# Kernel optimization log

Hardware: AMD Instinct MI355X
Metric: run time of the kernel (lower is better)

## Reference

```python
import jax, jax.numpy as jnp
import numpy as np

D_MODEL = 512
NUM_HEADS = 8
D_QKV = D_MODEL // NUM_HEADS  # 64
CAPACITY = 2  # EUNN tunable-style rotation layers per step
B = 2
L = 256


def setup_inputs() -> dict:
    key = jax.random.key(0)
    ks = jax.random.split(key, 16)
    f = jnp.float32
    x_q = jax.random.normal(ks[0], (B, L, D_MODEL), f)
    x_k = jax.random.normal(ks[1], (B, L, D_MODEL), f)
    x_v = jax.random.normal(ks[2], (B, L, D_MODEL), f)
    mask = jnp.zeros((B, 1, L, L), f)
    s = 1.0 / np.sqrt(D_MODEL).astype(np.float32)
    Wq = jax.random.normal(ks[3], (D_MODEL, D_MODEL), f) * s
    Wk = jax.random.normal(ks[4], (D_MODEL, D_MODEL), f) * s
    Wv = jax.random.normal(ks[5], (D_MODEL, D_MODEL), f) * s
    Wo = jax.random.normal(ks[6], (D_MODEL, D_MODEL), f) * s
    bq = jnp.zeros((D_MODEL,), f); bk = jnp.zeros((D_MODEL,), f)
    bv = jnp.zeros((D_MODEL,), f); bo = jnp.zeros((D_MODEL,), f)
    pi = np.float32(np.pi)
    theta = jax.random.uniform(ks[7], (NUM_HEADS, CAPACITY, D_QKV // 2), f, -pi, pi)
    phi = jax.random.uniform(ks[8], (NUM_HEADS, CAPACITY, D_QKV // 2), f, -pi, pi)
    sw = 1.0 / np.sqrt(D_QKV).astype(np.float32)
    Win_re = jax.random.normal(ks[9], (NUM_HEADS, D_QKV, D_QKV), f) * sw
    Win_im = jax.random.normal(ks[10], (NUM_HEADS, D_QKV, D_QKV), f) * sw
    rnn_bias = jax.random.normal(ks[11], (NUM_HEADS, D_QKV), f) * 0.01
    return dict(x_q=x_q, x_k=x_k, x_v=x_v, mask=mask, Wq=Wq, bq=bq, Wk=Wk, bk=bk,
                Wv=Wv, bv=bv, Wo=Wo, bo=bo, theta=theta, phi=phi,
                Win_re=Win_re, Win_im=Win_im, rnn_bias=rnn_bias)


def _apply_unitary(h, theta, phi):
    # h: [B,H,Q,d] complex64. EUNN unitary = product of Givens-rotation layers,
    # alternating even pairings (0,1),(2,3),.. and odd pairings via roll.
    for c in range(theta.shape[1]):
        if c % 2 == 1:
            h = jnp.roll(h, -1, axis=-1)
        sh = h.shape
        hp = h.reshape(sh[:-1] + (sh[-1] // 2, 2))
        a, b = hp[..., 0], hp[..., 1]
        cs = jnp.cos(theta[:, c, :])[None, :, None, :]
        sn = jnpp_sin = jnp.sin(theta[:, c, :])[None, :, None, :]
        ph = jnp.exp(1j * phi[:, c, :].astype(jnp.complex64))[None, :, None, :]
        na = cs * a - (sn * ph) * b
        nb = (sn * jnp.conj(ph)) * a + cs * b
        h = jnp.stack([na, nb], axis=-1).reshape(sh)
        if c % 2 == 1:
            h = jnp.roll(h, 1, axis=-1)
    return h


def _modrelu(z, b):
    m = jnp.abs(z)
    scale = jax.nn.relu(m + b) / (m + 1e-5)
    return z * scale.astype(z.dtype)


def _forward(x_q, x_k, x_v, mask, Wq, bq, Wk, bk, Wv, bv, Wo, bo,
             theta, phi, Win_re, Win_im, rnn_bias):
    Bm, Lq, _ = x_q.shape
    def heads(x):
        return x.reshape(Bm, -1, NUM_HEADS, D_QKV).transpose(0, 2, 1, 3)
    q = heads(x_q @ Wq + bq)   # [B,H,Lq,d]
    k = heads(x_k @ Wk + bk)   # [B,H,Lk,d]
    v = heads(x_v @ Wv + bv)   # [B,H,Lk,d]
    logits = jnp.einsum('bhqd,bhkd->bhqk', q, k) / jnp.sqrt(jnp.float32(D_QKV))
    logits = logits - jnp.where(mask == 1.0, jnp.inf, mask)
    attn = jax.nn.softmax(logits, axis=-1)  # [B,H,Lq,Lk]
    Win = (Win_re + 1j * Win_im).astype(jnp.complex64)  # [H,d,d]
    bb = rnn_bias[None, :, None, :]
    def step(h, xs):
        a_t, v_t = xs                              # [B,H,Q], [B,H,d]
        x_t = a_t[..., None] * v_t[:, :, None, :]  # [B,H,Q,d] streamed weighted value
        wx = jnp.einsum('bhqd,hde->bhqe', x_t.astype(jnp.complex64), Win)
        return _modrelu(_apply_unitary(h, theta, phi) + wx, bb), None
    h0 = jnp.zeros((Bm, NUM_HEADS, Lq, D_QKV), jnp.complex64)
    xs = (attn.transpose(3, 0, 1, 2), v.transpose(2, 0, 1, 3))
    hT, _ = jax.lax.scan(step, h0, xs)
    rnn_out = jnp.real(hT)  # [B,H,Lq,d] -- TF takes final RNN state, real part
    out = rnn_out.transpose(0, 2, 1, 3).reshape(Bm, Lq, D_MODEL) @ Wo + bo
    return out, attn


def reference(x_q, x_k, x_v, mask, Wq, bq, Wk, bk, Wv, bv, Wo, bo,
              theta, phi, Win_re, Win_im, rnn_bias):
    return _forward(x_q, x_k, x_v, mask, Wq, bq, Wk, bk, Wv, bv, Wo, bo,
                    theta, phi, Win_re, Win_im, rnn_bias)
```

## Files before the change

kernel.cpp:

```cpp
#include <hip/hip_runtime.h>
#include <math.h>

#define NB 2
#define NL 256
#define DM 512
#define NH 8
#define DQ 64

typedef float v2f __attribute__((ext_vector_type(2)));

#if __has_builtin(__builtin_elementwise_fma)
__device__ __forceinline__ v2f fmav(v2f a, v2f b, v2f c) {
    return __builtin_elementwise_fma(a, b, c);
}
#else
__device__ __forceinline__ v2f fmav(v2f a, v2f b, v2f c) {
    v2f r; r.x = fmaf(a.x, b.x, c.x); r.y = fmaf(a.y, b.y, c.y); return r;
}
#endif
__device__ __forceinline__ v2f swapv(v2f a) {
    return __builtin_shufflevector(a, a, 1, 0);
}

__global__ __launch_bounds__(256) void qkv_gemm(
    const float* __restrict__ xq, const float* __restrict__ xk,
    const float* __restrict__ xv,
    const float* __restrict__ Wq, const float* __restrict__ Wk,
    const float* __restrict__ Wv,
    const float* __restrict__ bq, const float* __restrict__ bk,
    const float* __restrict__ bv,
    const float* __restrict__ Wre, const float* __restrict__ Wim,
    float* __restrict__ q, float* __restrict__ kT, float2* __restrict__ u)
{
    int z = blockIdx.z;
    const float* X = (z == 0) ? xq : (z == 1) ? xk : xv;
    const float* W = (z == 0) ? Wq : (z == 1) ? Wk : Wv;
    const float* bias = (z == 0) ? bq : (z == 1) ? bk : bv;

    __shared__ float As[32][33];
    __shared__ float Bs[32][68];

    int tid = threadIdx.x;
    int tx = tid & 15, ty = tid >> 4;
    int m0 = blockIdx.y * 32, n0 = blockIdx.x * 64;

    int ar = tid >> 3, ac4 = (tid & 7) * 4;
    int br = tid >> 4, bc4 = (tid & 15) * 4;
    const float* Aptr = X + (m0 + ar) * 512 + ac4;
    const float* Bptr0 = W + br * 512 + n0 + bc4;
    const float* Bptr1 = W + (br + 16) * 512 + n0 + bc4;

    float acc[2][4] = {};

    float4 aR = *(const float4*)(Aptr);
    float4 bR0 = *(const float4*)(Bptr0);
    float4 bR1 = *(const float4*)(Bptr1);

    for (int k0 = 0; k0 < 512; k0 += 32) {
        As[ac4 + 0][ar] = aR.x; As[ac4 + 1][ar] = aR.y;
        As[ac4 + 2][ar] = aR.z; As[ac4 + 3][ar] = aR.w;
        *(float4*)&Bs[br][bc4] = bR0;
        *(float4*)&Bs[br + 16][bc4] = bR1;
        __syncthreads();

        if (k0 + 32 < 512) {
            aR  = *(const float4*)(Aptr + k0 + 32);
            bR0 = *(const float4*)(Bptr0 + (k0 + 32) * 512);
            bR1 = *(const float4*)(Bptr1 + (k0 + 32) * 512);
        }

        #pragma unroll
        for (int kk = 0; kk < 32; kk++) {
            float a0 = As[kk][ty * 2 + 0];
            float a1 = As[kk][ty * 2 + 1];
            float4 bb = *(const float4*)&Bs[kk][tx * 4];
            acc[0][0] += a0 * bb.x; acc[0][1] += a0 * bb.y;
            acc[0][2] += a0 * bb.z; acc[0][3] += a0 * bb.w;
            acc[1][0] += a1 * bb.x; acc[1][1] += a1 * bb.y;
            acc[1][2] += a1 * bb.z; acc[1][3] += a1 * bb.w;
        }
        __syncthreads();
    }

    if (z < 2) {
        float* O = (z == 0) ? q : kT;
        #pragma unroll
        for (int i = 0; i < 2; i++) {
            int m = m0 + ty * 2 + i;
            int b = m >> 8, l = m & 255;
            #pragma unroll
            for (int j = 0; j < 4; j++) {
                int n = n0 + tx * 4 + j;
                int h = n >> 6, d = n & 63;
                float val = acc[i][j] + bias[n];
                if (z == 1)
                    O[((b * NH + h) * DQ + d) * NL + l] = val;
                else
                    O[((b * NH + h) * NL + l) * DQ + d] = val;
            }
        }
    } else {
        int h = blockIdx.x;
        int b = m0 >> 8;
        #pragma unroll
        for (int i = 0; i < 2; i++)
            #pragma unroll
            for (int j = 0; j < 4; j++)
                Bs[ty * 2 + i][tx * 4 + j] = acc[i][j] + bias[n0 + tx * 4 + j];
        __syncthreads();

        int r0 = ty * 2, c4 = tx * 4;
        float ur[2][4] = {}, ui[2][4] = {};
        const float* wr = Wre + h * 4096 + c4;
        const float* wi = Wim + h * 4096 + c4;
        #pragma unroll 4
        for (int d = 0; d < 64; d++) {
            float v0 = Bs[r0][d];
            float v1 = Bs[r0 + 1][d];
            float4 wre = *(const float4*)(wr + d * 64);
            float4 wim = *(const float4*)(wi + d * 64);
            ur[0][0] += v0 * wre.x; ur[0][1] += v0 * wre.y;
            ur[0][2] += v0 * wre.z; ur[0][3] += v0 * wre.w;
            ui[0][0] += v0 * wim.x; ui[0][1] += v0 * wim.y;
            ui[0][2] += v0 * wim.z; ui[0][3] += v0 * wim.w;
            ur[1][0] += v1 * wre.x; ur[1][1] += v1 * wre.y;
            ur[1][2] += v1 * wre.z; ur[1][3] += v1 * wre.w;
            ui[1][0] += v1 * wim.x; ui[1][1] += v1 * wim.y;
            ui[1][2] += v1 * wim.z; ui[1][3] += v1 * wim.w;
        }
        #pragma unroll
        for (int i = 0; i < 2; i++) {
            int l = (m0 & 255) + r0 + i;
            float2* up = u + ((size_t)(b * NH + h) * NL + l) * DQ + c4;
            #pragma unroll
            for (int j = 0; j < 4; j++)
                up[j] = make_float2(ur[i][j], ui[i][j]);
        }
    }
}

__device__ __forceinline__ float dpp_row_ror1(float x) {
    return __int_as_float(__builtin_amdgcn_mov_dpp(__float_as_int(x), 0x121, 0xF, 0xF, true));
}
__device__ __forceinline__ float dpp_row_rol1(float x) {
    return __int_as_float(__builtin_amdgcn_mov_dpp(__float_as_int(x), 0x12F, 0xF, 0xF, true));
}

__device__ __forceinline__ v2f mdr(v2f z, float bv) {
    float mm = z.x * z.x + z.y * z.y;
    float m = __builtin_amdgcn_sqrtf(mm);
    float sc = fmaxf(m + bv, 0.f) * __builtin_amdgcn_rcpf(m + 1e-5f);
    v2f s = {sc, sc};
    return z * s;
}

__global__ __launch_bounds__(64) void rnn_kernel(
    const float* __restrict__ q, const float* __restrict__ kT,
    const float* __restrict__ mask, float* __restrict__ attn_o,
    const float2* __restrict__ u,
    const float* __restrict__ theta, const float* __restrict__ phi,
    const float* __restrict__ rnn_bias, float* __restrict__ rnn_out)
{
    int lane = threadIdx.x;
    int blk = blockIdx.x;
    int qg = blk & 63;
    int h  = (blk >> 6) & 7;
    int b  = blk >> 9;

    int row = lane >> 4;
    int p   = lane & 15;

    __shared__ float qs[4][68];
    __shared__ float arow[4][260];

    {
        const float4* qsrc = (const float4*)(q + ((size_t)(b * NH + h) * NL + qg * 4) * DQ);
        float4 f4 = qsrc[lane];
        *(float4*)&qs[lane >> 4][(lane & 15) * 4] = f4;
    }
    __syncthreads();

    float l[4][4];
    {
        const float* kp = kT + (size_t)((b * NH + h) * DQ) * NL + lane;
        float acc[4][4] = {};
        #pragma unroll
        for (int d4 = 0; d4 < 16; d4++) {
            float kv[4][4];
            #pragma unroll
            for (int kk = 0; kk < 4; kk++)
                #pragma unroll
                for (int i = 0; i < 4; i++)
                    kv[kk][i] = kp[(size_t)(d4 * 4 + i) * NL + kk * 64];
            #pragma unroll
            for (int r = 0; r < 4; r++) {
                float4 qv = *(const float4*)&qs[r][d4 * 4];
                #pragma unroll
                for (int kk = 0; kk < 4; kk++)
                    acc[r][kk] += qv.x * kv[kk][0] + qv.y * kv[kk][1]
                                + qv.z * kv[kk][2] + qv.w * kv[kk][3];
            }
        }
        #pragma unroll
        for (int r = 0; r < 4; r++)
            #pragma unroll
            for (int kk = 0; kk < 4; kk++) {
                float mv = mask[(size_t)(b * NL + qg * 4 + r) * NL + lane + kk * 64];
                l[r][kk] = acc[r][kk] * 0.125f - ((mv == 1.0f) ? INFINITY : mv);
            }
        #pragma unroll
        for (int r = 0; r < 4; r++) {
            float mx = fmaxf(fmaxf(l[r][0], l[r][1]), fmaxf(l[r][2], l[r][3]));
            #pragma unroll
            for (int o = 32; o; o >>= 1) mx = fmaxf(mx, __shfl_xor(mx, o, 64));
            float s = __expf(l[r][0] - mx) + __expf(l[r][1] - mx)
                    + __expf(l[r][2] - mx) + __expf(l[r][3] - mx);
            #pragma unroll
            for (int o = 32; o; o >>= 1) s += __shfl_xor(s, o, 64);
            float rs = __builtin_amdgcn_rcpf(s);
            #pragma unroll
            for (int kk = 0; kk < 4; kk++) {
                float pv = __expf(l[r][kk] - mx) * rs;
                attn_o[((size_t)(b * NH + h) * NL + qg * 4 + r) * NL + lane + kk * 64] = pv;
                arow[r][lane + kk * 64] = pv;
            }
        }
    }
    __syncthreads();

    const float* tb = theta + h * 64;
    const float* pb = phi + h * 64;

    float thA = tb[2 * p], phA = pb[2 * p];
    float cA = cosf(thA), sA = sinf(thA), cpA = cosf(phA), spA = sinf(phA);
    float thB = tb[2 * p + 1], phB = pb[2 * p + 1];
    float cB = cosf(thB), sB = sinf(thB), cpB = cosf(phB), spB = sinf(phB);

    #define MKC(nm, Wr, Wi) v2f nm##rV = {(Wr), (Wr)}; v2f nm##iN = {-(Wi), (Wi)}
    MKC(WAa, -sA * cpA, -sA * spA);
    MKC(WAb,  sA * cpA, -sA * spA);
    MKC(WBa, -sB * cpB, -sB * spB);
    MKC(WBb,  sB * cpB, -sB * spB);
    v2f cAv = {cA, cA}, cBv = {cB, cB};

    int iL = (2 * p + 31) & 31;
    float thL = tb[32 + iL], phL = pb[32 + iL];
    float cL = cosf(thL), sL = sinf(thL);
    MKC(W1L,  sL * cosf(phL), -sL * sinf(phL));
    float thM = tb[32 + 2 * p], phM = pb[32 + 2 * p];
    float cM = cosf(thM), sM = sinf(thM), cpM = cosf(phM), spM = sinf(phM);
    MKC(W1M, -sM * cpM, -sM * spM);
    MKC(W2M,  sM * cpM, -sM * spM);
    float thR = tb[32 + 2 * p + 1], phR = pb[32 + 2 * p + 1];
    float cR = cosf(thR), sR = sinf(thR);
    MKC(W1R, -sR * cosf(phR), -sR * sinf(phR));
    v2f cLv = {cL, cL}, cMv = {cM, cM}, cRv = {cR, cR};
    #undef MKC

    float4 bias4 = *(const float4*)&rnn_bias[h * 64 + 4 * p];

    v2f e0 = {0.f, 0.f}, e1 = {0.f, 0.f}, e2 = {0.f, 0.f}, e3 = {0.f, 0.f};

    #define STEP(a_t, uA, uB) do {                                           \
        v2f atv = {(a_t), (a_t)};                                            \
        v2f u0 = {(uA).x, (uA).y}, u1 = {(uA).z, (uA).w};                    \
        v2f u2 = {(uB).x, (uB).y}, u3 = {(uB).z, (uB).w};                    \
        v2f g0 = fmav(cAv, e0, fmav(WAarV, e1, WAaiN * swapv(e1)));          \
        v2f g1 = fmav(cAv, e1, fmav(WAbrV, e0, WAbiN * swapv(e0)));          \
        v2f g2 = fmav(cBv, e2, fmav(WBarV, e3, WBaiN * swapv(e3)));          \
        v2f g3 = fmav(cBv, e3, fmav(WBbrV, e2, WBbiN * swapv(e2)));          \
        v2f gl, gr;                                                          \
        gl.x = dpp_row_ror1(g3.x); gl.y = dpp_row_ror1(g3.y);                \
        gr.x = dpp_row_rol1(g0.x); gr.y = dpp_row_rol1(g0.y);                \
        v2f z0 = fmav(cLv, g0, fmav(W1LrV, gl, fmav(W1LiN, swapv(gl), atv * u0))); \
        v2f z1 = fmav(cMv, g1, fmav(W1MrV, g2, fmav(W1MiN, swapv(g2), atv * u1))); \
        v2f z2 = fmav(cMv, g2, fmav(W2MrV, g1, fmav(W2MiN, swapv(g1), atv * u2))); \
        v2f z3 = fmav(cRv, g3, fmav(W1RrV, gr, fmav(W1RiN, swapv(gr), atv * u3))); \
        e0 = mdr(z0, bias4.x); e1 = mdr(z1, bias4.y);                        \
        e2 = mdr(z2, bias4.z); e3 = mdr(z3, bias4.w);                        \
    } while (0)

    const float4* up4 = (const float4*)(u + (size_t)((b * NH + h) * NL) * DQ) + 2 * p;

    float4 Ua[8], Ub[8];
    float4 aa, ab;
    #pragma unroll
    for (int i = 0; i < 8; i++) Ua[i] = up4[(i >> 1) * 32 + (i & 1)];
    aa = *(const float4*)&arow[row][0];

    for (int c = 0; c < 64; c += 2) {
        const float4* upn = up4 + (c + 1) * 128;
        #pragma unroll
        for (int i = 0; i < 8; i++) Ub[i] = upn[(i >> 1) * 32 + (i & 1)];
        ab = *(const float4*)&arow[row][(c + 1) * 4];

        STEP(aa.x, Ua[0], Ua[1]);
        STEP(aa.y, Ua[2], Ua[3]);
        STEP(aa.z, Ua[4], Ua[5]);
        STEP(aa.w, Ua[6], Ua[7]);

        if (c + 2 < 64) {
            const float4* upn2 = up4 + (c + 2) * 128;
            #pragma unroll
            for (int i = 0; i < 8; i++) Ua[i] = upn2[(i >> 1) * 32 + (i & 1)];
            aa = *(const float4*)&arow[row][(c + 2) * 4];
        }

        STEP(ab.x, Ub[0], Ub[1]);
        STEP(ab.y, Ub[2], Ub[3]);
        STEP(ab.z, Ub[4], Ub[5]);
        STEP(ab.w, Ub[6], Ub[7]);
    }
    #undef STEP

    int qi = qg * 4 + row;
    float4 o4 = {e0.x, e1.x, e2.x, e3.x};
    *(float4*)&rnn_out[(size_t)(b * NL + qi) * DM + h * DQ + 4 * p] = o4;
}

__global__ __launch_bounds__(256) void out_gemm(
    const float* __restrict__ A, const float* __restrict__ W,
    const float* __restrict__ bias, float* __restrict__ C)
{
    __shared__ float As[32][17];
    __shared__ float Bs[32][68];

    int tid = threadIdx.x;
    int tx = tid & 15, ty = tid >> 4;
    int m0 = blockIdx.y * 16, n0 = blockIdx.x * 64;

    int ar = tid >> 4, ac2 = (tid & 15) * 2;
    int br = tid >> 4, bc4 = (tid & 15) * 4;
    const float* Aptr = A + (m0 + ar) * 512 + ac2;
    const float* Bptr0 = W + br * 512 + n0 + bc4;
    const float* Bptr1 = W + (br + 16) * 512 + n0 + bc4;

    float acc[4] = {};

    float2 aR = *(const float2*)(Aptr);
    float4 bR0 = *(const float4*)(Bptr0);
    float4 bR1 = *(const float4*)(Bptr1);

    for (int k0 = 0; k0 < 512; k0 += 32) {
        As[ac2 + 0][ar] = aR.x; As[ac2 + 1][ar] = aR.y;
        *(float4*)&Bs[br][bc4] = bR0;
        *(float4*)&Bs[br + 16][bc4] = bR1;
        __syncthreads();

        if (k0 + 32 < 512) {
            aR  = *(const float2*)(Aptr + k0 + 32);
            bR0 = *(const float4*)(Bptr0 + (k0 + 32) * 512);
            bR1 = *(const float4*)(Bptr1 + (k0 + 32) * 512);
        }

        #pragma unroll
        for (int kk = 0; kk < 32; kk++) {
            float a = As[kk][ty];
            float4 bb = *(const float4*)&Bs[kk][tx * 4];
            acc[0] += a * bb.x; acc[1] += a * bb.y;
            acc[2] += a * bb.z; acc[3] += a * bb.w;
        }
        __syncthreads();
    }

    int m = m0 + ty;
    #pragma unroll
    for (int j = 0; j < 4; j++) {
        int n = n0 + tx * 4 + j;
        C[m * 512 + n] = acc[j] + bias[n];
    }
}

extern "C" void kernel_launch(void* const* d_in, const int* in_sizes, int n_in,
                              void* d_out, int out_size, void* d_ws, size_t ws_size,
                              hipStream_t stream)
{
    const float* x_q  = (const float*)d_in[0];
    const float* x_k  = (const float*)d_in[1];
    const float* x_v  = (const float*)d_in[2];
    const float* mask = (const float*)d_in[3];
    const float* Wq   = (const float*)d_in[4];
    const float* bq   = (const float*)d_in[5];
    const float* Wk   = (const float*)d_in[6];
    const float* bk   = (const float*)d_in[7];
    const float* Wv   = (const float*)d_in[8];
    const float* bv   = (const float*)d_in[9];
    const float* Wo   = (const float*)d_in[10];
    const float* bo   = (const float*)d_in[11];
    const float* theta= (const float*)d_in[12];
    const float* phi  = (const float*)d_in[13];
    const float* Wre  = (const float*)d_in[14];
    const float* Wim  = (const float*)d_in[15];
    const float* rb   = (const float*)d_in[16];

    float* ws = (float*)d_ws;
    float*  q_ws    = ws;
    float*  kT_ws   = ws + 262144;
    float2* u_ws    = (float2*)(ws + 524288);
    float*  rnn_o   = ws + 1048576;

    float* out_o  = (float*)d_out;
    float* attn_o = out_o + NB * NL * DM;

    qkv_gemm<<<dim3(8, 16, 3), 256, 0, stream>>>(
        x_q, x_k, x_v, Wq, Wk, Wv, bq, bk, bv, Wre, Wim,
        q_ws, kT_ws, u_ws);

    rnn_kernel<<<dim3(1024), 64, 0, stream>>>(
        q_ws, kT_ws, mask, attn_o, u_ws, theta, phi, rb, rnn_o);

    out_gemm<<<dim3(8, 32), 256, 0, stream>>>(rnn_o, Wo, bo, out_o);
}
```

Baseline: 182.0 us.

## Halve per-lane RNN state and double blocks in recurrent kernel

The RNN kernel now handles 2 query rows per 64-lane block instead of 4, so each lane carries 2 complex state elements (one Givens pair) rather than 4. The grid doubles to 2048 blocks. The cross-lane shift for the odd rotation layer becomes two DPP quad-perm moves over interleaved lanes instead of a row rotate. The aim is to shorten the serial 256-step per-lane dependency chain and raise parallelism, at the cost of recomputing the QK logits and loading K once per 2 rows instead of once per 4.

```diff
diff --git a/kernel.cpp b/kernel.cpp
--- a/kernel.cpp
+++ b/kernel.cpp
@@ -139,11 +139,15 @@
     }
 }
 
-__device__ __forceinline__ float dpp_row_ror1(float x) {
-    return __int_as_float(__builtin_amdgcn_mov_dpp(__float_as_int(x), 0x121, 0xF, 0xF, true));
-}
-__device__ __forceinline__ float dpp_row_rol1(float x) {
-    return __int_as_float(__builtin_amdgcn_mov_dpp(__float_as_int(x), 0x12F, 0xF, 0xF, true));
+__device__ __forceinline__ float rot_up2(float x) {
+    int v = __builtin_amdgcn_mov_dpp(__float_as_int(x), 0x134, 0xF, 0xF, true);
+    v = __builtin_amdgcn_mov_dpp(v, 0x134, 0xF, 0xF, true);
+    return __int_as_float(v);
+}
+__device__ __forceinline__ float rot_dn2(float x) {
+    int v = __builtin_amdgcn_mov_dpp(__float_as_int(x), 0x13C, 0xF, 0xF, true);
+    v = __builtin_amdgcn_mov_dpp(v, 0x13C, 0xF, 0xF, true);
+    return __int_as_float(v);
 }
 
 __device__ __forceinline__ v2f mdr(v2f z, float bv) {
@@ -163,27 +167,28 @@
 {
     int lane = threadIdx.x;
     int blk = blockIdx.x;
-    int qg = blk & 63;
-    int h  = (blk >> 6) & 7;
-    int b  = blk >> 9;
-
-    int row = lane >> 4;
-    int p   = lane & 15;
-
-    __shared__ float qs[4][68];
-    __shared__ float arow[4][260];
+    int qg = blk & 127;
+    int h  = (blk >> 7) & 7;
+    int b  = blk >> 10;
+
+    int row = lane & 1;
+    int p   = lane >> 1;
+
+    __shared__ float qs[2][68];
+    __shared__ float arow[2][260];
 
     {
-        const float4* qsrc = (const float4*)(q + ((size_t)(b * NH + h) * NL + qg * 4) * DQ);
-        float4 f4 = qsrc[lane];
-        *(float4*)&qs[lane >> 4][(lane & 15) * 4] = f4;
+        const float4* qsrc = (const float4*)(q + ((size_t)(b * NH + h) * NL + qg * 2) * DQ);
+        if (lane < 32) {
+            float4 f4 = qsrc[lane];
+            *(float4*)&qs[lane >> 4][(lane & 15) * 4] = f4;
+        }
     }
     __syncthreads();
 
-    float l[4][4];
     {
         const float* kp = kT + (size_t)((b * NH + h) * DQ) * NL + lane;
-        float acc[4][4] = {};
+        float acc[2][4] = {};
         #pragma unroll
         for (int d4 = 0; d4 < 16; d4++) {
             float kv[4][4];
@@ -193,7 +198,7 @@
                 for (int i = 0; i < 4; i++)
                     kv[kk][i] = kp[(size_t)(d4 * 4 + i) * NL + kk * 64];
             #pragma unroll
-            for (int r = 0; r < 4; r++) {
+            for (int r = 0; r < 2; r++) {
                 float4 qv = *(const float4*)&qs[r][d4 * 4];
                 #pragma unroll
                 for (int kk = 0; kk < 4; kk++)
@@ -201,15 +206,16 @@
                                 + qv.z * kv[kk][2] + qv.w * kv[kk][3];
             }
         }
-        #pragma unroll
-        for (int r = 0; r < 4; r++)
+        float l[2][4];
+        #pragma unroll
+        for (int r = 0; r < 2; r++)
             #pragma unroll
             for (int kk = 0; kk < 4; kk++) {
-                float mv = mask[(size_t)(b * NL + qg * 4 + r) * NL + lane + kk * 64];
+                float mv = mask[(size_t)(b * NL + qg * 2 + r) * NL + lane + kk * 64];
                 l[r][kk] = acc[r][kk] * 0.125f - ((mv == 1.0f) ? INFINITY : mv);
             }
         #pragma unroll
-        for (int r = 0; r < 4; r++) {
+        for (int r = 0; r < 2; r++) {
             float mx = fmaxf(fmaxf(l[r][0], l[r][1]), fmaxf(l[r][2], l[r][3]));
             #pragma unroll
             for (int o = 32; o; o >>= 1) mx = fmaxf(mx, __shfl_xor(mx, o, 64));
@@ -221,7 +227,7 @@
             #pragma unroll
             for (int kk = 0; kk < 4; kk++) {
                 float pv = __expf(l[r][kk] - mx) * rs;
-                attn_o[((size_t)(b * NH + h) * NL + qg * 4 + r) * NL + lane + kk * 64] = pv;
+                attn_o[((size_t)(b * NH + h) * NL + qg * 2 + r) * NL + lane + kk * 64] = pv;
                 arow[r][lane + kk * 64] = pv;
             }
         }
@@ -231,91 +237,78 @@
     const float* tb = theta + h * 64;
     const float* pb = phi + h * 64;
 
-    float thA = tb[2 * p], phA = pb[2 * p];
-    float cA = cosf(thA), sA = sinf(thA), cpA = cosf(phA), spA = sinf(phA);
-    float thB = tb[2 * p + 1], phB = pb[2 * p + 1];
-    float cB = cosf(thB), sB = sinf(thB), cpB = cosf(phB), spB = sinf(phB);
-
     #define MKC(nm, Wr, Wi) v2f nm##rV = {(Wr), (Wr)}; v2f nm##iN = {-(Wi), (Wi)}
-    MKC(WAa, -sA * cpA, -sA * spA);
-    MKC(WAb,  sA * cpA, -sA * spA);
-    MKC(WBa, -sB * cpB, -sB * spB);
-    MKC(WBb,  sB * cpB, -sB * spB);
-    v2f cAv = {cA, cA}, cBv = {cB, cB};
-
-    int iL = (2 * p + 31) & 31;
-    float thL = tb[32 + iL], phL = pb[32 + iL];
-    float cL = cosf(thL), sL = sinf(thL);
-    MKC(W1L,  sL * cosf(phL), -sL * sinf(phL));
-    float thM = tb[32 + 2 * p], phM = pb[32 + 2 * p];
-    float cM = cosf(thM), sM = sinf(thM), cpM = cosf(phM), spM = sinf(phM);
-    MKC(W1M, -sM * cpM, -sM * spM);
-    MKC(W2M,  sM * cpM, -sM * spM);
-    float thR = tb[32 + 2 * p + 1], phR = pb[32 + 2 * p + 1];
-    float cR = cosf(thR), sR = sinf(thR);
-    MKC(W1R, -sR * cosf(phR), -sR * sinf(phR));
-    v2f cLv = {cL, cL}, cMv = {cM, cM}, cRv = {cR, cR};
+
+    float th0 = tb[p], ph0 = pb[p];
+    float c0 = cosf(th0), s0 = sinf(th0), cp0 = cosf(ph0), sp0 = sinf(ph0);
+    MKC(WSa, -s0 * cp0, -s0 * sp0);
+    MKC(WSb,  s0 * cp0, -s0 * sp0);
+    v2f c0v = {c0, c0};
+
+    int iE = (p + 31) & 31;
+    float thE = tb[32 + iE], phE = pb[32 + iE];
+    float cE = cosf(thE), sE = sinf(thE);
+    MKC(W1E,  sE * cosf(phE), -sE * sinf(phE));
+    v2f cEv = {cE, cE};
+    float thO = tb[32 + p], phO = pb[32 + p];
+    float cO = cosf(thO), sO = sinf(thO);
+    MKC(W1O, -sO * cosf(phO), -sO * sinf(phO));
+    v2f cOv = {cO, cO};
     #undef MKC
 
-    float4 bias4 = *(const float4*)&rnn_bias[h * 64 + 4 * p];
-
-    v2f e0 = {0.f, 0.f}, e1 = {0.f, 0.f}, e2 = {0.f, 0.f}, e3 = {0.f, 0.f};
-
-    #define STEP(a_t, uA, uB) do {                                           \
+    float2 bias2 = *(const float2*)&rnn_bias[h * 64 + 2 * p];
+
+    v2f ea = {0.f, 0.f}, eb = {0.f, 0.f};
+
+    #define STEP(a_t, uu) do {                                               \
         v2f atv = {(a_t), (a_t)};                                            \
-        v2f u0 = {(uA).x, (uA).y}, u1 = {(uA).z, (uA).w};                    \
-        v2f u2 = {(uB).x, (uB).y}, u3 = {(uB).z, (uB).w};                    \
-        v2f g0 = fmav(cAv, e0, fmav(WAarV, e1, WAaiN * swapv(e1)));          \
-        v2f g1 = fmav(cAv, e1, fmav(WAbrV, e0, WAbiN * swapv(e0)));          \
-        v2f g2 = fmav(cBv, e2, fmav(WBarV, e3, WBaiN * swapv(e3)));          \
-        v2f g3 = fmav(cBv, e3, fmav(WBbrV, e2, WBbiN * swapv(e2)));          \
+        v2f u0 = {(uu).x, (uu).y}, u1 = {(uu).z, (uu).w};                    \
+        v2f ga = fmav(c0v, ea, fmav(WSarV, eb, WSaiN * swapv(eb)));          \
+        v2f gb = fmav(c0v, eb, fmav(WSbrV, ea, WSbiN * swapv(ea)));          \
         v2f gl, gr;                                                          \
-        gl.x = dpp_row_ror1(g3.x); gl.y = dpp_row_ror1(g3.y);                \
-        gr.x = dpp_row_rol1(g0.x); gr.y = dpp_row_rol1(g0.y);                \
-        v2f z0 = fmav(cLv, g0, fmav(W1LrV, gl, fmav(W1LiN, swapv(gl), atv * u0))); \
-        v2f z1 = fmav(cMv, g1, fmav(W1MrV, g2, fmav(W1MiN, swapv(g2), atv * u1))); \
-        v2f z2 = fmav(cMv, g2, fmav(W2MrV, g1, fmav(W2MiN, swapv(g1), atv * u2))); \
-        v2f z3 = fmav(cRv, g3, fmav(W1RrV, gr, fmav(W1RiN, swapv(gr), atv * u3))); \
-        e0 = mdr(z0, bias4.x); e1 = mdr(z1, bias4.y);                        \
-        e2 = mdr(z2, bias4.z); e3 = mdr(z3, bias4.w);                        \
+        gl.x = rot_dn2(gb.x); gl.y = rot_dn2(gb.y);                          \
+        gr.x = rot_up2(ga.x); gr.y = rot_up2(ga.y);                          \
+        v2f za = fmav(cEv, ga, fmav(W1ErV, gl, fmav(W1EiN, swapv(gl), atv * u0))); \
+        v2f zb = fmav(cOv, gb, fmav(W1OrV, gr, fmav(W1OiN, swapv(gr), atv * u1))); \
+        ea = mdr(za, bias2.x); eb = mdr(zb, bias2.y);                        \
     } while (0)
 
-    const float4* up4 = (const float4*)(u + (size_t)((b * NH + h) * NL) * DQ) + 2 * p;
-
-    float4 Ua[8], Ub[8];
+    const float4* up4 = (const float4*)(u + (size_t)((b * NH + h) * NL) * DQ) + p;
+
+    float4 Ua[4], Ub[4];
     float4 aa, ab;
     #pragma unroll
-    for (int i = 0; i < 8; i++) Ua[i] = up4[(i >> 1) * 32 + (i & 1)];
+    for (int i = 0; i < 4; i++) Ua[i] = up4[i * 32];
     aa = *(const float4*)&arow[row][0];
 
     for (int c = 0; c < 64; c += 2) {
         const float4* upn = up4 + (c + 1) * 128;
         #pragma unroll
-        for (int i = 0; i < 8; i++) Ub[i] = upn[(i >> 1) * 32 + (i & 1)];
+        for (int i = 0; i < 4; i++) Ub[i] = upn[i * 32];
         ab = *(const float4*)&arow[row][(c + 1) * 4];
 
-        STEP(aa.x, Ua[0], Ua[1]);
-        STEP(aa.y, Ua[2], Ua[3]);
-        STEP(aa.z, Ua[4], Ua[5]);
-        STEP(aa.w, Ua[6], Ua[7]);
+        STEP(aa.x, Ua[0]);
+        STEP(aa.y, Ua[1]);
+        STEP(aa.z, Ua[2]);
+        STEP(aa.w, Ua[3]);
 
         if (c + 2 < 64) {
             const float4* upn2 = up4 + (c + 2) * 128;
             #pragma unroll
-            for (int i = 0; i < 8; i++) Ua[i] = upn2[(i >> 1) * 32 + (i & 1)];
+            for (int i = 0; i < 4; i++) Ua[i] = upn2[i * 32];
             aa = *(const float4*)&arow[row][(c + 2) * 4];
         }
 
-        STEP(ab.x, Ub[0], Ub[1]);
-        STEP(ab.y, Ub[2], Ub[3]);
-        STEP(ab.z, Ub[4], Ub[5]);
-        STEP(ab.w, Ub[6], Ub[7]);
+        STEP(ab.x, Ub[0]);
+        STEP(ab.y, Ub[1]);
+        STEP(ab.z, Ub[2]);
+        STEP(ab.w, Ub[3]);
     }
     #undef STEP
 
-    int qi = qg * 4 + row;
-    float4 o4 = {e0.x, e1.x, e2.x, e3.x};
-    *(float4*)&rnn_out[(size_t)(b * NL + qi) * DM + h * DQ + 4 * p] = o4;
+    int qi = qg * 2 + row;
+    *(float2*)&rnn_out[(size_t)(b * NL + qi) * DM + h * DQ + 2 * p] =
+        make_float2(ea.x, eb.x);
 }
 
 __global__ __launch_bounds__(256) void out_gemm(
@@ -406,7 +399,7 @@
         x_q, x_k, x_v, Wq, Wk, Wv, bq, bk, bv, Wre, Wim,
         q_ws, kT_ws, u_ws);
 
-    rnn_kernel<<<dim3(1024), 64, 0, stream>>>(
+    rnn_kernel<<<dim3(2048), 64, 0, stream>>>(
         q_ws, kT_ws, mask, attn_o, u_ws, theta, phi, rb, rnn_o);
 
     out_gemm<<<dim3(8, 32), 256, 0, stream>>>(rnn_o, Wo, bo, out_o);
```

Result: no change. 184.7 us (+1.5%).
